# Performance work log

Hardware: AMD Instinct MI355X
Metric: run time of the kernel (lower is better)

The kernel has to match this reference:

```python
import jax, jax.numpy as jnp
import numpy as np

NOISE = 0.02
P_CONST = 1.0
NUM_LAYERS = 7


def setup_inputs() -> dict:
    key = jax.random.key(0)
    k1, k2, k3, k4 = jax.random.split(key, 4)
    B, Nt, K, L = 2048, 64, 40, NUM_LAYERS
    sqrtP = np.sqrt(P_CONST)
    return {
        'H_real': jax.random.normal(k1, (B, Nt, K), dtype=jnp.float32),
        'H_imag': jax.random.normal(k2, (B, Nt, K), dtype=jnp.float32),
        'eta': jnp.ones((L,), dtype=jnp.float32) * (0.1 / sqrtP),
        'U': jax.random.normal(k3, (L, Nt, Nt), dtype=jnp.float32) * (0.01 / sqrtP),
        'b': jax.random.normal(k4, (L, Nt, K), dtype=jnp.float32) * (0.01 / sqrtP),
    }


def _rate_total(Wr, Wi, Hc):
    # sum over batch of (sum_k log2(1+sinr_k) - power_penalty)
    W = Wr + 1j * Wi                                   # [B,Nt,K] complex
    HW = jnp.einsum('bnk,bnl->bkl', jnp.conj(Hc), W)   # [B,K,K]
    pw = jnp.abs(HW) ** 2                              # |h_k^H w_l|^2
    desired = jnp.diagonal(pw, axis1=1, axis2=2)       # [B,K]
    interference = pw.sum(axis=2) - desired
    sinr = desired / (interference + NOISE)
    rates = jnp.log2(1.0 + sinr).sum()
    power = jnp.sum(Wr * Wr + Wi * Wi, axis=(1, 2))    # ||W||_F^2 per batch
    penalty = jnp.mean((power - P_CONST) ** 2) * 0.01
    B = Wr.shape[0]
    return rates - B * penalty


def reference(H_real, H_imag, eta, U, b):
    Hc = H_real + 1j * H_imag
    B, Nt, K = H_real.shape
    Wr = jnp.zeros((B, Nt, K), dtype=jnp.float32)
    Wi = jnp.zeros((B, Nt, K), dtype=jnp.float32)
    grad_fn = jax.grad(_rate_total, argnums=(0, 1))
    for t in range(NUM_LAYERS):
        g_r, g_i = grad_fn(Wr, Wi, Hc)                 # torch grad: dL/dx + i dL/dy
        Ug_r = jnp.einsum('nm,bmk->bnk', U[t], g_r)
        Ug_i = jnp.einsum('nm,bmk->bnk', U[t], g_i)
        step_r = Ug_r - Ug_i
        step_i = Ug_i + Ug_r
        Wr = Wr - eta[t] * step_r + b[t]
        Wi = Wi - eta[t] * step_i
    # final power normalization
    norm = jnp.sqrt(jnp.sum(Wr * Wr + Wi * Wi, axis=(1, 2), keepdims=True))
    scale = jnp.sqrt(P_CONST) / (norm + 1e-6)
    Wr = Wr * scale
    Wi = Wi * scale
    return Wr + 1j * Wi
```

## Files before the change

kernel.cpp:

```cpp
#include <hip/hip_runtime.h>
#include <math.h>

typedef _Float16 h16;
typedef __attribute__((ext_vector_type(2))) _Float16 h16x2;
typedef __attribute__((ext_vector_type(4))) _Float16 h16x4;
typedef __attribute__((ext_vector_type(8))) _Float16 h16x8;
typedef __attribute__((ext_vector_type(4))) float f32x4;

#define NBATCH 2048
#define NT 64
#define KK 40
#define NL 7
#define SIGMA 0.02f
#define INVLN2 1.4426950408889634f

#define RA   0
#define RB   (48*128)
#define HCK  (2*48*128)
#define HNC  (HCK + 48*128)
#define UOF  (HNC + 64*128)
#define LDSH (UOF + 64*64)

#define SWZ(row, c)  ((c) ^ (((row)&7)<<3))
#define SWZW(row, c) ((c) ^ (((row)&15)<<3))
#define MFMA16(a,b,c) __builtin_amdgcn_mfma_f32_16x16x32_f16((a),(b),(c),0,0,0)

static __device__ __forceinline__ float DOT2(h16x2 a, h16x2 b, float c) {
#if __has_builtin(__builtin_amdgcn_fdot2)
    return __builtin_amdgcn_fdot2(a, b, c, false);
#else
    return fmaf((float)a.x, (float)b.x, fmaf((float)a.y, (float)b.y, c));
#endif
}
static __device__ __forceinline__ h16x2 PK(float x, float y) {
    h16x2 r; r.x = (h16)x; r.y = (h16)y; return r;
}
static __device__ __forceinline__ h16x8 conjA(h16x8 v) {
    union { h16x8 h; unsigned u[4]; } x; x.h = v;
    #pragma unroll
    for (int i=0;i<4;++i){ unsigned t=x.u[i]; t=(t>>16)|(t<<16); x.u[i]=t^0x80000000u; }
    return x.h;
}
static __device__ __forceinline__ h16x8 imB(h16x8 v) {
    union { h16x8 h; unsigned u[4]; } x; x.h = v;
    #pragma unroll
    for (int i=0;i<4;++i){ unsigned t=x.u[i]; t=(t>>16)|(t<<16); x.u[i]=t^0x00008000u; }
    return x.h;
}

__global__ __launch_bounds__(256, 2) void gpnet_kernel(
    const float* __restrict__ gHr, const float* __restrict__ gHi,
    const float* __restrict__ gEta, const float* __restrict__ gU,
    const float* __restrict__ gB, float* __restrict__ gOut, int outFloats)
{
    __shared__ __align__(16) h16 sh[LDSH];
    __shared__ float sRed[4];

    const int tid = threadIdx.x;
    const int wv  = tid >> 6;
    const int ln  = tid & 63;
    const int col = ln & 15;
    const int g   = ln >> 4;

    const int bb = blockIdx.x;
    const float* hr = gHr + (size_t)bb * NT * KK;
    const float* hi = gHi + (size_t)bb * NT * KK;

    for (int i = tid; i < 512; i += 256) {
        *(h16x2*)(sh + RA  + 40*128 + 2*i) = PK(0.f, 0.f);
        *(h16x2*)(sh + HCK + 40*128 + 2*i) = PK(0.f, 0.f);
    }
    for (int i = tid; i < 512; i += 256) {
        int n = i >> 3, c = 80 + 2*(i & 7);
        *(h16x2*)(sh + HNC + n*128 + SWZ(n, c)) = PK(0.f, 0.f);
    }
    for (int i = tid; i < NT*KK; i += 256) {
        int n = i / KK, k = i % KK;
        float xr = hr[i], xi = hi[i];
        h16x2 p = PK(xr, xi);
        *(h16x2*)(sh + HCK + k*128 + SWZW(k, 2*n)) = p;
        *(h16x2*)(sh + HNC + n*128 + SWZ(n, 2*k)) = p;
        *(h16x2*)(sh + RA  + k*128 + SWZW(k, 2*n)) = PK(gB[i], 0.f);
    }
    float Wr[3][4], Wi[3][4];
    float ps = 0.f;
    #pragma unroll
    for (int ct = 0; ct < 3; ++ct)
        #pragma unroll
        for (int r = 0; r < 4; ++r) {
            int n = 16*wv + 4*g + r, l = col + 16*ct;
            float b0 = (l < KK) ? gB[n*KK + l] : 0.f;
            Wr[ct][r] = b0; Wi[ct][r] = 0.f;
            ps += b0 * b0;
        }
    #pragma unroll
    for (int off = 32; off; off >>= 1) ps += __shfl_down(ps, off, 64);
    if (ln == 0) sRed[wv] = ps;
    __syncthreads();

    for (int t = 1; t < NL; ++t) {
        const int P = (t & 1) ? RA : RB;
        const int Q = (t & 1) ? RB : RA;
        const int GREo = P, GIMo = P + 48*64;

        const float pw   = sRed[0] + sRed[1] + sRed[2] + sRed[3];
        const float cpen = 0.04f * (pw - 1.0f);
        const float etat = gEta[t];

        float breg[3][4];
        #pragma unroll
        for (int ct = 0; ct < 3; ++ct)
            #pragma unroll
            for (int r = 0; r < 4; ++r) {
                int n = 16*wv + 4*g + r, l = col + 16*ct;
                breg[ct][r] = (l < KK) ? gB[(size_t)t*NT*KK + n*KK + l] : 0.f;
            }

        if (wv < 3) {
            f32x4 aRe[3], aIm[3];
            #pragma unroll
            for (int rt = 0; rt < 3; ++rt) { aRe[rt] = (f32x4){0.f,0.f,0.f,0.f}; aIm[rt] = (f32x4){0.f,0.f,0.f,0.f}; }
            const int kcol = col + 16*wv;
            #pragma unroll
            for (int q = 0; q < 4; ++q) {
                h16x8 bf = *(const h16x8*)(sh + HCK + kcol*128 + SWZW(kcol, g*8 + 32*q));
                #pragma unroll
                for (int rt = 0; rt < 3; ++rt) {
                    int lrow = col + 16*rt;
                    h16x8 af = *(const h16x8*)(sh + P + lrow*128 + SWZW(lrow, g*8 + 32*q));
                    aRe[rt] = MFMA16(af, bf, aRe[rt]);
                    aIm[rt] = MFMA16(conjA(af), bf, aIm[rt]);
                }
            }
            #pragma unroll
            for (int rt = 0; rt < 3; ++rt)
                #pragma unroll
                for (int r = 0; r < 4; ++r) {
                    int l = 16*rt + 4*g + r;
                    *(h16x2*)(sh + Q + l*128 + SWZ(l, 2*kcol)) =
                        PK(aRe[rt][r], aIm[rt][r]);
                }
        } else {
            const float2* u2 = (const float2*)(gU + (size_t)t * NT * NT);
            #pragma unroll 8
            for (int j = 0; j < 32; ++j) {
                int e2 = j*64 + ln;
                float2 v = u2[e2];
                int n = e2 >> 5, m2 = (e2 & 31) * 2;
                *(h16x2*)(sh + UOF + n*64 + SWZ(n, m2)) = PK(v.x, v.y);
            }
        }
        __syncthreads();

        if (tid < 160) {
            const int k = tid >> 2, q = tid & 3;
            h16x2 va[10];
            #pragma unroll
            for (int ii = 0; ii < 10; ++ii)
                va[ii] = *(const h16x2*)(sh + Q + (q*10+ii)*128 + SWZ(q*10+ii, 2*k));
            float rs = 0.f, dd = 0.f;
            #pragma unroll
            for (int ii = 0; ii < 10; ++ii) rs = DOT2(va[ii], va[ii], rs);
            const int dk = k - q*10;
            if (dk >= 0 && dk < 10) dd = DOT2(va[dk], va[dk], 0.f);
            rs += __shfl_xor(rs, 1, 64); rs += __shfl_xor(rs, 2, 64);
            dd += __shfl_xor(dd, 1, 64); dd += __shfl_xor(dd, 2, 64);
            float T  = rs + SIGMA, Is = rs - dd + SIGMA;
            float cA_ = 2.f * INVLN2 / T;
            float cC_ = -2.f * INVLN2 * dd / (Is * T);
            #pragma unroll
            for (int ii = 0; ii < 10; ++ii) {
                int l = q*10 + ii;
                float c = (l == k) ? cA_ : cC_;
                *(h16x2*)(sh + Q + l*128 + SWZ(l, 2*k)) =
                    PK((float)va[ii].x * c, -(float)va[ii].y * c);
            }
        }
        __syncthreads();

        f32x4 gRe[3], gIm[3];
        #pragma unroll
        for (int ct = 0; ct < 3; ++ct) { gRe[ct] = (f32x4){0.f,0.f,0.f,0.f}; gIm[ct] = (f32x4){0.f,0.f,0.f,0.f}; }
        {
            const int nrow = col + 16*wv;
            #pragma unroll
            for (int q = 0; q < 3; ++q) {
                h16x8 af = *(const h16x8*)(sh + HNC + nrow*128 + SWZ(nrow, g*8 + 32*q));
                #pragma unroll
                for (int ct = 0; ct < 3; ++ct) {
                    int lr = col + 16*ct;
                    h16x8 bf = *(const h16x8*)(sh + Q + lr*128 + SWZ(lr, g*8 + 32*q));
                    gRe[ct] = MFMA16(af, bf, gRe[ct]);
                    gIm[ct] = MFMA16(af, imB(bf), gIm[ct]);
                }
            }
        }
        {
            const int n0w = 16*wv + 4*g;
            #pragma unroll
            for (int ct = 0; ct < 3; ++ct) {
                int l = col + 16*ct;
                h16x4 g4, q4;
                #pragma unroll
                for (int r = 0; r < 4; ++r) {
                    g4[r] = (h16)(gRe[ct][r] - cpen * Wr[ct][r]);
                    q4[r] = (h16)(gIm[ct][r] - cpen * Wi[ct][r]);
                }
                *(h16x4*)(sh + GREo + l*64 + SWZ(l, n0w)) = g4;
                *(h16x4*)(sh + GIMo + l*64 + SWZ(l, n0w)) = q4;
            }
        }
        __syncthreads();

        f32x4 cRe[3], cIm[3];
        #pragma unroll
        for (int ct = 0; ct < 3; ++ct) { cRe[ct] = (f32x4){0.f,0.f,0.f,0.f}; cIm[ct] = (f32x4){0.f,0.f,0.f,0.f}; }
        {
            const int nrow = col + 16*wv;
            #pragma unroll
            for (int q = 0; q < 2; ++q) {
                h16x8 af = *(const h16x8*)(sh + UOF + nrow*64 + SWZ(nrow, g*8 + 32*q));
                #pragma unroll
                for (int ct = 0; ct < 3; ++ct) {
                    const int l = col + 16*ct;
                    h16x8 fre = *(const h16x8*)(sh + GREo + l*64 + SWZ(l, g*8 + 32*q));
                    h16x8 fim = *(const h16x8*)(sh + GIMo + l*64 + SWZ(l, g*8 + 32*q));
                    cRe[ct] = MFMA16(af, fre, cRe[ct]);
                    cIm[ct] = MFMA16(af, fim, cIm[ct]);
                }
            }
        }
        float ps2 = 0.f;
        {
            const int n0w = 16*wv + 4*g;
            #pragma unroll
            for (int ct = 0; ct < 3; ++ct) {
                int l = col + 16*ct;
                h16x8 wvv;
                #pragma unroll
                for (int r = 0; r < 4; ++r) {
                    float ur = cRe[ct][r], ui = cIm[ct][r];
                    float wr = Wr[ct][r] - etat*(ur - ui) + breg[ct][r];
                    float wi = Wi[ct][r] - etat*(ui + ur);
                    Wr[ct][r] = wr; Wi[ct][r] = wi;
                    wvv[2*r]   = (h16)wr;
                    wvv[2*r+1] = (h16)wi;
                    if (l < KK) ps2 += wr*wr + wi*wi;
                }
                if (l < KK)
                    *(h16x8*)(sh + Q + l*128 + SWZW(l, 2*n0w)) = wvv;
            }
            h16x4 z4; z4[0] = (h16)0.f; z4[1] = (h16)0.f; z4[2] = (h16)0.f; z4[3] = (h16)0.f;
            *(h16x4*)(sh + Q + 40*128 + 4*tid) = z4;
        }
        #pragma unroll
        for (int off = 32; off; off >>= 1) ps2 += __shfl_down(ps2, off, 64);
        if (ln == 0) sRed[wv] = ps2;
        __syncthreads();
    }

    const float pwf   = sRed[0] + sRed[1] + sRed[2] + sRed[3];
    const float scale = 1.0f / (sqrtf(pwf) + 1e-6f);

    if (outFloats >= 2 * NBATCH * NT * KK) {
        float2* ob = (float2*)(gOut + (size_t)bb * NT * KK * 2);
        #pragma unroll
        for (int ct = 0; ct < 3; ++ct)
            #pragma unroll
            for (int r = 0; r < 4; ++r) {
                int n = 16*wv + 4*g + r, l = col + 16*ct;
                if (l < KK) {
                    float2 v; v.x = Wr[ct][r]*scale; v.y = Wi[ct][r]*scale;
                    ob[n*KK + l] = v;
                }
            }
    } else {
        float* ob = gOut + (size_t)bb * NT * KK;
        #pragma unroll
        for (int ct = 0; ct < 3; ++ct)
            #pragma unroll
            for (int r = 0; r < 4; ++r) {
                int n = 16*wv + 4*g + r, l = col + 16*ct;
                if (l < KK) ob[n*KK + l] = Wr[ct][r] * scale;
            }
    }
}

extern "C" void kernel_launch(void* const* d_in, const int* in_sizes, int n_in,
                              void* d_out, int out_size, void* d_ws, size_t ws_size,
                              hipStream_t stream) {
    (void)in_sizes; (void)n_in; (void)d_ws; (void)ws_size;
    const float* Hr  = (const float*)d_in[0];
    const float* Hi  = (const float*)d_in[1];
    const float* eta = (const float*)d_in[2];
    const float* U   = (const float*)d_in[3];
    const float* b   = (const float*)d_in[4];
    float* out = (float*)d_out;
    gpnet_kernel<<<NBATCH, 256, 0, stream>>>(Hr, Hi, eta, U, b, out, out_size);
}
```

Measured before the change: 114.2 us.

## Keep H and U MFMA operands in registers, shrink LDS, raise occupancy

The per-row H operand (HNC) and the per-layer U matrix (UOF) now load straight from global memory into registers as packed fp16 MFMA A-fragments, so they no longer need staging in shared memory. This removes about 24 KB of LDS and lets launch bounds ask for 3 blocks per CU instead of 2. It also drops the separate U-staging branch in wave 3 and skips the W write-back on the final layer. In exchange every wave issues its own uncoalesced float4 global loads for U each layer, and register pressure rises, which could cause spills under the tighter launch bound.

```diff
diff --git a/kernel.cpp b/kernel.cpp
--- a/kernel.cpp
+++ b/kernel.cpp
@@ -17,9 +17,7 @@
 #define RA   0
 #define RB   (48*128)
 #define HCK  (2*48*128)
-#define HNC  (HCK + 48*128)
-#define UOF  (HNC + 64*128)
-#define LDSH (UOF + 64*64)
+#define LDSH (HCK + 48*128)
 
 #define SWZ(row, c)  ((c) ^ (((row)&7)<<3))
 #define SWZW(row, c) ((c) ^ (((row)&15)<<3))
@@ -47,8 +45,14 @@
     for (int i=0;i<4;++i){ unsigned t=x.u[i]; t=(t>>16)|(t<<16); x.u[i]=t^0x00008000u; }
     return x.h;
 }
-
-__global__ __launch_bounds__(256, 2) void gpnet_kernel(
+static __device__ __forceinline__ h16x8 packRI(float4 a, float4 b) {
+    h16x8 v;
+    v[0]=(h16)a.x; v[1]=(h16)b.x; v[2]=(h16)a.y; v[3]=(h16)b.y;
+    v[4]=(h16)a.z; v[5]=(h16)b.z; v[6]=(h16)a.w; v[7]=(h16)b.w;
+    return v;
+}
+
+__global__ __launch_bounds__(256, 3) void gpnet_kernel(
     const float* __restrict__ gHr, const float* __restrict__ gHi,
     const float* __restrict__ gEta, const float* __restrict__ gU,
     const float* __restrict__ gB, float* __restrict__ gOut, int outFloats)
@@ -70,16 +74,9 @@
         *(h16x2*)(sh + RA  + 40*128 + 2*i) = PK(0.f, 0.f);
         *(h16x2*)(sh + HCK + 40*128 + 2*i) = PK(0.f, 0.f);
     }
-    for (int i = tid; i < 512; i += 256) {
-        int n = i >> 3, c = 80 + 2*(i & 7);
-        *(h16x2*)(sh + HNC + n*128 + SWZ(n, c)) = PK(0.f, 0.f);
-    }
     for (int i = tid; i < NT*KK; i += 256) {
         int n = i / KK, k = i % KK;
-        float xr = hr[i], xi = hi[i];
-        h16x2 p = PK(xr, xi);
-        *(h16x2*)(sh + HCK + k*128 + SWZW(k, 2*n)) = p;
-        *(h16x2*)(sh + HNC + n*128 + SWZ(n, 2*k)) = p;
+        *(h16x2*)(sh + HCK + k*128 + SWZW(k, 2*n)) = PK(hr[i], hi[i]);
         *(h16x2*)(sh + RA  + k*128 + SWZW(k, 2*n)) = PK(gB[i], 0.f);
     }
     float Wr[3][4], Wi[3][4];
@@ -96,6 +93,25 @@
     #pragma unroll
     for (int off = 32; off; off >>= 1) ps += __shfl_down(ps, off, 64);
     if (ln == 0) sRed[wv] = ps;
+
+    h16x8 paf[3];
+    {
+        const int nrow = col + 16*wv;
+        h16x8 z;
+        #pragma unroll
+        for (int j = 0; j < 8; ++j) z[j] = (h16)0.f;
+        #pragma unroll
+        for (int q = 0; q < 3; ++q) {
+            const int kb = g*4 + 16*q;
+            if (q < 2 || g < 2) {
+                float4 a = *(const float4*)(hr + nrow*KK + kb);
+                float4 b = *(const float4*)(hi + nrow*KK + kb);
+                paf[q] = packRI(a, b);
+            } else {
+                paf[q] = z;
+            }
+        }
+    }
     __syncthreads();
 
     for (int t = 1; t < NL; ++t) {
@@ -115,6 +131,21 @@
                 int n = 16*wv + 4*g + r, l = col + 16*ct;
                 breg[ct][r] = (l < KK) ? gB[(size_t)t*NT*KK + n*KK + l] : 0.f;
             }
+        h16x8 puf[2];
+        {
+            const int nrow = col + 16*wv;
+            const float* ut = gU + (size_t)t * NT * NT + nrow*NT;
+            #pragma unroll
+            for (int q = 0; q < 2; ++q) {
+                const int mb = g*8 + 32*q;
+                float4 a = *(const float4*)(ut + mb);
+                float4 b = *(const float4*)(ut + mb + 4);
+                h16x8 v;
+                v[0]=(h16)a.x; v[1]=(h16)a.y; v[2]=(h16)a.z; v[3]=(h16)a.w;
+                v[4]=(h16)b.x; v[5]=(h16)b.y; v[6]=(h16)b.z; v[7]=(h16)b.w;
+                puf[q] = v;
+            }
+        }
 
         if (wv < 3) {
             f32x4 aRe[3], aIm[3];
@@ -140,15 +171,6 @@
                     *(h16x2*)(sh + Q + l*128 + SWZ(l, 2*kcol)) =
                         PK(aRe[rt][r], aIm[rt][r]);
                 }
-        } else {
-            const float2* u2 = (const float2*)(gU + (size_t)t * NT * NT);
-            #pragma unroll 8
-            for (int j = 0; j < 32; ++j) {
-                int e2 = j*64 + ln;
-                float2 v = u2[e2];
-                int n = e2 >> 5, m2 = (e2 & 31) * 2;
-                *(h16x2*)(sh + UOF + n*64 + SWZ(n, m2)) = PK(v.x, v.y);
-            }
         }
         __syncthreads();
 
@@ -182,10 +204,9 @@
         #pragma unroll
         for (int ct = 0; ct < 3; ++ct) { gRe[ct] = (f32x4){0.f,0.f,0.f,0.f}; gIm[ct] = (f32x4){0.f,0.f,0.f,0.f}; }
         {
-            const int nrow = col + 16*wv;
             #pragma unroll
             for (int q = 0; q < 3; ++q) {
-                h16x8 af = *(const h16x8*)(sh + HNC + nrow*128 + SWZ(nrow, g*8 + 32*q));
+                h16x8 af = paf[q];
                 #pragma unroll
                 for (int ct = 0; ct < 3; ++ct) {
                     int lr = col + 16*ct;
@@ -216,10 +237,9 @@
         #pragma unroll
         for (int ct = 0; ct < 3; ++ct) { cRe[ct] = (f32x4){0.f,0.f,0.f,0.f}; cIm[ct] = (f32x4){0.f,0.f,0.f,0.f}; }
         {
-            const int nrow = col + 16*wv;
             #pragma unroll
             for (int q = 0; q < 2; ++q) {
-                h16x8 af = *(const h16x8*)(sh + UOF + nrow*64 + SWZ(nrow, g*8 + 32*q));
+                h16x8 af = puf[q];
                 #pragma unroll
                 for (int ct = 0; ct < 3; ++ct) {
                     const int l = col + 16*ct;
@@ -247,11 +267,13 @@
                     wvv[2*r+1] = (h16)wi;
                     if (l < KK) ps2 += wr*wr + wi*wi;
                 }
-                if (l < KK)
+                if (t < NL-1 && l < KK)
                     *(h16x8*)(sh + Q + l*128 + SWZW(l, 2*n0w)) = wvv;
             }
-            h16x4 z4; z4[0] = (h16)0.f; z4[1] = (h16)0.f; z4[2] = (h16)0.f; z4[3] = (h16)0.f;
-            *(h16x4*)(sh + Q + 40*128 + 4*tid) = z4;
+            if (t < NL-1) {
+                h16x4 z4; z4[0] = (h16)0.f; z4[1] = (h16)0.f; z4[2] = (h16)0.f; z4[3] = (h16)0.f;
+                *(h16x4*)(sh + Q + 40*128 + 4*tid) = z4;
+            }
         }
         #pragma unroll
         for (int off = 32; off; off >>= 1) ps2 += __shfl_down(ps2, off, 64);
```

Result: slower. 184.4 us (+61.4%).

## Shrink LDS footprint to raise occupancy; keep H^T fragments in registers

Applied to the files above, without the earlier changes.

Removes the padded 48-row buffers and the separate HNC (n-major H) copy from shared memory. The A-operand fragments for the gradient MFMA are built once from the HCK copy and kept in registers. Out-of-range rows are clamped to row 0 and their results discarded, so the zero-padding stores go away, and launch bounds are raised to three blocks per CU. The smaller LDS allows more resident blocks, at the cost of extra registers and some clamping and masking logic.

```diff
diff --git a/kernel.cpp b/kernel.cpp
--- a/kernel.cpp
+++ b/kernel.cpp
@@ -15,10 +15,9 @@
 #define INVLN2 1.4426950408889634f
 
 #define RA   0
-#define RB   (48*128)
-#define HCK  (2*48*128)
-#define HNC  (HCK + 48*128)
-#define UOF  (HNC + 64*128)
+#define RB   (40*128)
+#define HCK  (2*40*128)
+#define UOF  (3*40*128)
 #define LDSH (UOF + 64*64)
 
 #define SWZ(row, c)  ((c) ^ (((row)&7)<<3))
@@ -47,8 +46,14 @@
     for (int i=0;i<4;++i){ unsigned t=x.u[i]; t=(t>>16)|(t<<16); x.u[i]=t^0x00008000u; }
     return x.h;
 }
-
-__global__ __launch_bounds__(256, 2) void gpnet_kernel(
+static __device__ __forceinline__ h16x8 zsel(h16x8 v, bool p) {
+    union { h16x8 h; unsigned u[4]; } x; x.h = v;
+    #pragma unroll
+    for (int i=0;i<4;++i) x.u[i] = p ? x.u[i] : 0u;
+    return x.h;
+}
+
+__global__ __launch_bounds__(256, 3) void gpnet_kernel(
     const float* __restrict__ gHr, const float* __restrict__ gHi,
     const float* __restrict__ gEta, const float* __restrict__ gU,
     const float* __restrict__ gB, float* __restrict__ gOut, int outFloats)
@@ -66,20 +71,9 @@
     const float* hr = gHr + (size_t)bb * NT * KK;
     const float* hi = gHi + (size_t)bb * NT * KK;
 
-    for (int i = tid; i < 512; i += 256) {
-        *(h16x2*)(sh + RA  + 40*128 + 2*i) = PK(0.f, 0.f);
-        *(h16x2*)(sh + HCK + 40*128 + 2*i) = PK(0.f, 0.f);
-    }
-    for (int i = tid; i < 512; i += 256) {
-        int n = i >> 3, c = 80 + 2*(i & 7);
-        *(h16x2*)(sh + HNC + n*128 + SWZ(n, c)) = PK(0.f, 0.f);
-    }
     for (int i = tid; i < NT*KK; i += 256) {
         int n = i / KK, k = i % KK;
-        float xr = hr[i], xi = hi[i];
-        h16x2 p = PK(xr, xi);
-        *(h16x2*)(sh + HCK + k*128 + SWZW(k, 2*n)) = p;
-        *(h16x2*)(sh + HNC + n*128 + SWZ(n, 2*k)) = p;
+        *(h16x2*)(sh + HCK + k*128 + SWZW(k, 2*n)) = PK(hr[i], hi[i]);
         *(h16x2*)(sh + RA  + k*128 + SWZW(k, 2*n)) = PK(gB[i], 0.f);
     }
     float Wr[3][4], Wi[3][4];
@@ -98,10 +92,30 @@
     if (ln == 0) sRed[wv] = ps;
     __syncthreads();
 
+    h16x8 paf[3];
+    {
+        const int nrow = col + 16*wv;
+        #pragma unroll
+        for (int q = 0; q < 3; ++q) {
+            h16x8 v;
+            #pragma unroll
+            for (int j = 0; j < 8; ++j) v[j] = (h16)0.f;
+            if (q < 2 || g < 2) {
+                const int kb = g*4 + 16*q;
+                #pragma unroll
+                for (int i = 0; i < 4; ++i) {
+                    h16x2 p = *(const h16x2*)(sh + HCK + (kb+i)*128 + SWZW(kb+i, 2*nrow));
+                    v[2*i] = p.x; v[2*i+1] = p.y;
+                }
+            }
+            paf[q] = v;
+        }
+    }
+
     for (int t = 1; t < NL; ++t) {
         const int P = (t & 1) ? RA : RB;
         const int Q = (t & 1) ? RB : RA;
-        const int GREo = P, GIMo = P + 48*64;
+        const int GREo = P, GIMo = P + 40*64;
 
         const float pw   = sRed[0] + sRed[1] + sRed[2] + sRed[3];
         const float cpen = 0.04f * (pw - 1.0f);
@@ -121,13 +135,17 @@
             #pragma unroll
             for (int rt = 0; rt < 3; ++rt) { aRe[rt] = (f32x4){0.f,0.f,0.f,0.f}; aIm[rt] = (f32x4){0.f,0.f,0.f,0.f}; }
             const int kcol = col + 16*wv;
+            const bool vK = (kcol < KK);
+            const int kC = vK ? kcol : 0;
             #pragma unroll
             for (int q = 0; q < 4; ++q) {
-                h16x8 bf = *(const h16x8*)(sh + HCK + kcol*128 + SWZW(kcol, g*8 + 32*q));
+                h16x8 bf = *(const h16x8*)(sh + HCK + kC*128 + SWZW(kC, g*8 + 32*q));
+                bf = zsel(bf, vK);
                 #pragma unroll
                 for (int rt = 0; rt < 3; ++rt) {
                     int lrow = col + 16*rt;
-                    h16x8 af = *(const h16x8*)(sh + P + lrow*128 + SWZW(lrow, g*8 + 32*q));
+                    int lC = (lrow < KK) ? lrow : 0;
+                    h16x8 af = *(const h16x8*)(sh + P + lC*128 + SWZW(lC, g*8 + 32*q));
                     aRe[rt] = MFMA16(af, bf, aRe[rt]);
                     aIm[rt] = MFMA16(conjA(af), bf, aIm[rt]);
                 }
@@ -137,8 +155,9 @@
                 #pragma unroll
                 for (int r = 0; r < 4; ++r) {
                     int l = 16*rt + 4*g + r;
-                    *(h16x2*)(sh + Q + l*128 + SWZ(l, 2*kcol)) =
-                        PK(aRe[rt][r], aIm[rt][r]);
+                    if (l < KK)
+                        *(h16x2*)(sh + Q + l*128 + SWZ(l, 2*kcol)) =
+                            PK(aRe[rt][r], aIm[rt][r]);
                 }
         } else {
             const float2* u2 = (const float2*)(gU + (size_t)t * NT * NT);
@@ -182,14 +201,14 @@
         #pragma unroll
         for (int ct = 0; ct < 3; ++ct) { gRe[ct] = (f32x4){0.f,0.f,0.f,0.f}; gIm[ct] = (f32x4){0.f,0.f,0.f,0.f}; }
         {
-            const int nrow = col + 16*wv;
             #pragma unroll
             for (int q = 0; q < 3; ++q) {
-                h16x8 af = *(const h16x8*)(sh + HNC + nrow*128 + SWZ(nrow, g*8 + 32*q));
+                h16x8 af = paf[q];
                 #pragma unroll
                 for (int ct = 0; ct < 3; ++ct) {
                     int lr = col + 16*ct;
-                    h16x8 bf = *(const h16x8*)(sh + Q + lr*128 + SWZ(lr, g*8 + 32*q));
+                    int lrC = (lr < KK) ? lr : 0;
+                    h16x8 bf = *(const h16x8*)(sh + Q + lrC*128 + SWZ(lrC, g*8 + 32*q));
                     gRe[ct] = MFMA16(af, bf, gRe[ct]);
                     gIm[ct] = MFMA16(af, imB(bf), gIm[ct]);
                 }
@@ -200,14 +219,16 @@
             #pragma unroll
             for (int ct = 0; ct < 3; ++ct) {
                 int l = col + 16*ct;
-                h16x4 g4, q4;
-                #pragma unroll
-                for (int r = 0; r < 4; ++r) {
-                    g4[r] = (h16)(gRe[ct][r] - cpen * Wr[ct][r]);
-                    q4[r] = (h16)(gIm[ct][r] - cpen * Wi[ct][r]);
-                }
-                *(h16x4*)(sh + GREo + l*64 + SWZ(l, n0w)) = g4;
-                *(h16x4*)(sh + GIMo + l*64 + SWZ(l, n0w)) = q4;
+                if (l < KK) {
+                    h16x4 g4, q4;
+                    #pragma unroll
+                    for (int r = 0; r < 4; ++r) {
+                        g4[r] = (h16)(gRe[ct][r] - cpen * Wr[ct][r]);
+                        q4[r] = (h16)(gIm[ct][r] - cpen * Wi[ct][r]);
+                    }
+                    *(h16x4*)(sh + GREo + l*64 + SWZ(l, n0w)) = g4;
+                    *(h16x4*)(sh + GIMo + l*64 + SWZ(l, n0w)) = q4;
+                }
             }
         }
         __syncthreads();
@@ -223,8 +244,9 @@
                 #pragma unroll
                 for (int ct = 0; ct < 3; ++ct) {
                     const int l = col + 16*ct;
-                    h16x8 fre = *(const h16x8*)(sh + GREo + l*64 + SWZ(l, g*8 + 32*q));
-                    h16x8 fim = *(const h16x8*)(sh + GIMo + l*64 + SWZ(l, g*8 + 32*q));
+                    const int lC = (l < KK) ? l : 0;
+                    h16x8 fre = *(const h16x8*)(sh + GREo + lC*64 + SWZ(lC, g*8 + 32*q));
+                    h16x8 fim = *(const h16x8*)(sh + GIMo + lC*64 + SWZ(lC, g*8 + 32*q));
                     cRe[ct] = MFMA16(af, fre, cRe[ct]);
                     cIm[ct] = MFMA16(af, fim, cIm[ct]);
                 }
@@ -247,11 +269,9 @@
                     wvv[2*r+1] = (h16)wi;
                     if (l < KK) ps2 += wr*wr + wi*wi;
                 }
-                if (l < KK)
+                if (t < NL-1 && l < KK)
                     *(h16x8*)(sh + Q + l*128 + SWZW(l, 2*n0w)) = wvv;
             }
-            h16x4 z4; z4[0] = (h16)0.f; z4[1] = (h16)0.f; z4[2] = (h16)0.f; z4[3] = (h16)0.f;
-            *(h16x4*)(sh + Q + 40*128 + 4*tid) = z4;
         }
         #pragma unroll
         for (int off = 32; off; off >>= 1) ps2 += __shfl_down(ps2, off, 64);
```

Result: slower. 241.8 us (+111.6%).
